# Kernel tuning notes

Measured on AMD Instinct MI355X. Metric: run time of the kernel, lower is better.

## Reference

```python
import jax, jax.numpy as jnp
import numpy as np

NEG_INF = -9e15
ALPHA = 0.2  # LeakyReLU negative slope

N, IN_F, OUT_F = 8192, 512, 64


def setup_inputs() -> dict:
    key = jax.random.key(0)
    k1, k2, k3, k4 = jax.random.split(key, 4)
    input = jax.random.normal(k1, (N, IN_F), dtype=jnp.float32)
    adj = jax.random.randint(k2, (N, N), 0, 2, dtype=jnp.int32)
    init_range = float(np.sqrt(6.0 / (IN_F + OUT_F)))
    W = jax.random.uniform(k3, (IN_F, OUT_F), dtype=jnp.float32,
                           minval=-init_range, maxval=init_range)
    a_range = float(np.sqrt(6.0 / (2 * OUT_F + 1)))
    a = jax.random.uniform(k4, (2 * OUT_F, 1), dtype=jnp.float32,
                           minval=-a_range, maxval=a_range)
    return {"input": input, "adj": adj, "W": W, "a": a}


def reference(input, adj, W, a):
    h = input @ W                      # [N, F']
    a_left, a_right = a[:OUT_F], a[OUT_F:]   # each [F', 1]
    att_l = h @ a_left                 # [N, 1]
    att_r = h @ a_right                # [N, 1]
    e = jax.nn.leaky_relu(att_l + att_r.T, negative_slope=ALPHA)  # [N, N]
    e = jnp.where(adj == 0, jnp.float32(NEG_INF), e)
    attention = jax.nn.softmax(e, axis=1)
    # dropout is identity in eval mode (training=False)
    h_prime = attention @ h            # [N, F']
    return jax.nn.elu(h_prime)         # concat=True -> ELU activation
```

## Files before the change

### kernel.cpp

```cpp
#include <hip/hip_runtime.h>
#include <stdint.h>

#define ALPHA 0.2f
#define LOG2E 1.44269504088896340736f

typedef __attribute__((ext_vector_type(8))) short bf16x8;
typedef __attribute__((ext_vector_type(4))) float f32x4;

__device__ __forceinline__ unsigned short f2bf(float f) {
    unsigned u = __builtin_bit_cast(unsigned, f);
    u += 0x7fffu + ((u >> 16) & 1u);
    return (unsigned short)(u >> 16);
}
__device__ __forceinline__ float bf2f(unsigned short h) {
    unsigned u = ((unsigned)h) << 16;
    return __builtin_bit_cast(float, u);
}
__device__ __forceinline__ unsigned f2ord(float f) {
    unsigned b = __builtin_bit_cast(unsigned, f);
    return (b & 0x80000000u) ? ~b : (b | 0x80000000u);
}
__device__ __forceinline__ float ord2f(unsigned k) {
    unsigned b = (k & 0x80000000u) ? (k & 0x7fffffffu) : ~k;
    return __builtin_bit_cast(float, b);
}

__global__ __launch_bounds__(256) void gat_pre(
    const float* __restrict__ input, const float* __restrict__ W,
    const float* __restrict__ a,
    float* __restrict__ attL, float* __restrict__ attR,
    unsigned short* __restrict__ hPack, unsigned* __restrict__ wsR)
{
    __shared__ float x_lds[16 * 512];
    __shared__ float h_lds[16 * 64];
    __shared__ unsigned rmax;
    const int tid = threadIdx.x;
    const int i0  = blockIdx.x * 16;
    if (tid == 0) rmax = 0u;

    {
        const float* src = input + (size_t)i0 * 512;
        #pragma unroll
        for (int u = 0; u < 8; ++u) {
            const int f = (u * 256 + tid) * 4;
            *(f32x4*)&x_lds[f] = *(const f32x4*)(src + f);
        }
    }
    __syncthreads();

    {
        const int c = tid & 63;
        const int w = tid >> 6;
        float acc[4] = {0.f, 0.f, 0.f, 0.f};
        const float* Wc = W + c;
        #pragma unroll 4
        for (int kk = 0; kk < 512; kk += 4) {
            const float w0 = Wc[(kk+0)*64], w1 = Wc[(kk+1)*64];
            const float w2 = Wc[(kk+2)*64], w3 = Wc[(kk+3)*64];
            #pragma unroll
            for (int ri = 0; ri < 4; ++ri) {
                const f32x4 x = *(const f32x4*)&x_lds[(w + 4*ri) * 512 + kk];
                acc[ri] += x.x * w0 + x.y * w1 + x.z * w2 + x.w * w3;
            }
        }
        #pragma unroll
        for (int ri = 0; ri < 4; ++ri)
            h_lds[(w + 4*ri) * 64 + c] = acc[ri];
    }
    __syncthreads();

    if (tid < 128) {
        const int row = tid >> 3;
        const int cs  = (tid & 7) * 8;
        float pL = 0.f, pR = 0.f;
        #pragma unroll
        for (int u = 0; u < 8; ++u) {
            const float hv = h_lds[row * 64 + cs + u];
            pL += hv * a[cs + u];
            pR += hv * a[64 + cs + u];
        }
        pL += __shfl_xor(pL, 1, 64); pR += __shfl_xor(pR, 1, 64);
        pL += __shfl_xor(pL, 2, 64); pR += __shfl_xor(pR, 2, 64);
        pL += __shfl_xor(pL, 4, 64); pR += __shfl_xor(pR, 4, 64);
        if ((tid & 7) == 0) {
            attL[i0 + row] = pL;
            attR[i0 + row] = pR;
            atomicMax(&rmax, f2ord(pR));
        }
    } else {
        const int t2   = tid - 128;
        const int g    = t2 >> 5;
        const int qq   = (t2 >> 4) & 1;
        const int m    = t2 & 15;
        const int jb   = blockIdx.x >> 1;
        const int half = blockIdx.x & 1;
        bf16x8 v;
        #pragma unroll
        for (int u = 0; u < 8; ++u)
            v[u] = (short)f2bf(h_lds[(qq * 8 + u) * 64 + g * 16 + m]);
        *(bf16x8*)&hPack[(size_t)(jb * 4 + g) * 512 + ((half * 2 + qq) * 16 + m) * 8] = v;
    }

    __syncthreads();
    if (tid == 0) atomicMax(wsR, rmax);
}

__global__ __launch_bounds__(256, 4) void gat_attn(
    const int* __restrict__ adj,
    const float* __restrict__ attL, const float* __restrict__ attR,
    const unsigned short* __restrict__ hPack, const unsigned* __restrict__ wsR,
    float* __restrict__ outAcc, float* __restrict__ lAcc)
{
    __shared__ unsigned smem[4096];
    __shared__ float l_lds[64];
    const int tid  = threadIdx.x;
    const int lane = tid & 63;
    const int wq   = tid >> 6;
    const int m    = lane & 15;
    const int quad = lane >> 4;
    const int ti   = blockIdx.x >> 2;
    const int q4   = blockIdx.x & 3;
    const int i0   = ti * 16;
    const int jc0  = q4 * 64 + wq * 16;

    {
        const int r    = tid >> 4;
        const int lidx = (tid & 3) * 16 + r;
        const int t    = (tid & 15) >> 2;
        unsigned char* bb = (unsigned char*)smem;
        const int* src = adj + (size_t)(i0 + r) * 8192 + q4 * 2048 + (tid & 15) * 8;
        #pragma unroll 4
        for (int it = 0; it < 16; ++it) {
            const int4 v0 = *(const int4*)(src + it * 128);
            const int4 v1 = *(const int4*)(src + it * 128 + 4);
            unsigned b = 0;
            b |= (v0.x != 0) << 0; b |= (v0.y != 0) << 1;
            b |= (v0.z != 0) << 2; b |= (v0.w != 0) << 3;
            b |= (v1.x != 0) << 4; b |= (v1.y != 0) << 5;
            b |= (v1.z != 0) << 6; b |= (v1.w != 0) << 7;
            bb[((((it >> 2) * 1024) + (it & 3) * 64 + lidx) << 2) + t] = (unsigned char)b;
        }
    }
    __syncthreads();

    unsigned abw[4];
    #pragma unroll
    for (int g4 = 0; g4 < 4; ++g4)
        abw[g4] = smem[wq * 1024 + g4 * 64 + lane];

    const float R   = ord2f(*wsR);
    const float a_l = attL[i0 + m];
    const float t0  = a_l + R;
    const float M   = fmaxf(t0, ALPHA * t0);
    const float mc  = M * LOG2E;

    const float*          ar_p = attR + jc0 * 32 + quad * 8;
    const unsigned short* hp_p = hPack + (size_t)jc0 * 4 * 512 + lane * 8;

    f32x4 acc[4];
    #pragma unroll
    for (int g = 0; g < 4; ++g) acc[g] = (f32x4){0.f, 0.f, 0.f, 0.f};
    float lsum = 0.f;

    #pragma unroll
    for (int jg = 0; jg < 4; ++jg) {
        const unsigned ab = abw[jg];
        #pragma unroll
        for (int t = 0; t < 4; ++t) {
            const int s = jg * 4 + t;
            const f32x4 r0 = *(const f32x4*)(ar_p + s * 32);
            const f32x4 r1 = *(const f32x4*)(ar_p + s * 32 + 4);
            bf16x8 B[4];
            #pragma unroll
            for (int g = 0; g < 4; ++g)
                B[g] = *(const bf16x8*)(hp_p + (size_t)(s * 4 + g) * 512);

            const unsigned bits = (ab >> (t * 8)) & 0xffu;
            const float tv[8] = { a_l + r0.x, a_l + r0.y, a_l + r0.z, a_l + r0.w,
                                  a_l + r1.x, a_l + r1.y, a_l + r1.z, a_l + r1.w };
            bf16x8 af;
            #pragma unroll
            for (int u = 0; u < 8; ++u) {
                const float e  = fmaxf(tv[u], ALPHA * tv[u]);
                const float pe = __builtin_amdgcn_exp2f(__builtin_fmaf(e, LOG2E, -mc));
                const float pv = (bits & (1u << u)) ? pe : 0.0f;
                const unsigned short pb = f2bf(pv);
                af[u] = (short)pb;
                lsum += bf2f(pb);
            }
            #pragma unroll
            for (int g = 0; g < 4; ++g)
                acc[g] = __builtin_amdgcn_mfma_f32_16x16x32_bf16(af, B[g], acc[g], 0, 0, 0);
        }
    }

    lsum += __shfl_xor(lsum, 16, 64);
    lsum += __shfl_xor(lsum, 32, 64);
    if (lane < 16) l_lds[wq * 16 + lane] = lsum;
    float* accf = (float*)smem;
    #pragma unroll
    for (int g = 0; g < 4; ++g)
        *(f32x4*)&accf[(wq * 64 + lane) * 16 + g * 4] = acc[g];
    __syncthreads();

    #pragma unroll
    for (int q = 0; q < 4; ++q) {
        const int e      = tid + q * 256;
        const int lane_e = e >> 4;
        const int k16    = e & 15;
        float s = 0.f;
        #pragma unroll
        for (int ww = 0; ww < 4; ++ww) s += accf[(ww * 64 + lane_e) * 16 + k16];
        const int row = (lane_e >> 4) * 4 + (k16 & 3);
        const int col = (k16 >> 2) * 16 + (lane_e & 15);
        unsafeAtomicAdd(&outAcc[(size_t)(i0 + row) * 64 + col], s);
    }
    if (tid < 16) {
        const float s = l_lds[tid] + l_lds[16 + tid] + l_lds[32 + tid] + l_lds[48 + tid];
        unsafeAtomicAdd(&lAcc[i0 + tid], s);
    }
}

__global__ __launch_bounds__(256) void gat_final(
    float* __restrict__ out, const float* __restrict__ lAcc)
{
    const int idx = blockIdx.x * 256 + threadIdx.x;
    const float v = out[idx] / lAcc[idx >> 6];
    out[idx] = v > 0.f ? v : (__builtin_amdgcn_exp2f(v * LOG2E) - 1.0f);
}

extern "C" void kernel_launch(void* const* d_in, const int* in_sizes, int n_in,
                              void* d_out, int out_size, void* d_ws, size_t ws_size,
                              hipStream_t stream) {
    const float* input = (const float*)d_in[0];
    const int*   adj   = (const int*)d_in[1];
    const float* W     = (const float*)d_in[2];
    const float* a     = (const float*)d_in[3];
    float* out = (float*)d_out;

    char* ws = (char*)d_ws;
    unsigned*       wsR   = (unsigned*)(ws + 0);
    float*          lAcc  = (float*)(ws + 4096);
    float*          attL  = (float*)(ws + 2134016);
    float*          attR  = (float*)(ws + 2166784);
    unsigned short* hPack = (unsigned short*)(ws + 2199552);

    hipMemsetAsync(d_out, 0, (size_t)out_size * sizeof(float), stream);
    hipMemsetAsync(d_ws, 0, 36864, stream);

    gat_pre  <<< 512, 256, 0, stream>>>(input, W, a, attL, attR, hPack, wsR);
    gat_attn <<<2048, 256, 0, stream>>>(adj, attL, attR, hPack, wsR, out, lAcc);
    gat_final<<<2048, 256, 0, stream>>>(out, lAcc);
}
```

Measured before the change: 419.3 us.

## Fuse normalization and ELU into attention kernel by giving each block full rows

Each attention block now processes all 8192 columns for its 16 rows using 8 waves, instead of splitting columns across 4 blocks. Partial results are reduced in LDS rather than with global atomics, and the softmax normalization and ELU are applied in place. This removes the output memset, the lAcc accumulator, the atomics and the separate final kernel. In exchange the grid has fewer, larger blocks and more registers per thread, which could reduce occupancy or cause spills under the 512x4 launch bound.

```diff
diff --git a/kernel.cpp b/kernel.cpp
--- a/kernel.cpp
+++ b/kernel.cpp
@@ -105,48 +105,49 @@
     if (tid == 0) atomicMax(wsR, rmax);
 }
 
-__global__ __launch_bounds__(256, 4) void gat_attn(
+__global__ __launch_bounds__(512, 4) void gat_attn(
     const int* __restrict__ adj,
     const float* __restrict__ attL, const float* __restrict__ attR,
     const unsigned short* __restrict__ hPack, const unsigned* __restrict__ wsR,
-    float* __restrict__ outAcc, float* __restrict__ lAcc)
+    float* __restrict__ out)
 {
-    __shared__ unsigned smem[4096];
-    __shared__ float l_lds[64];
+    __shared__ unsigned smem[8192];
+    __shared__ float l_lds[128];
     const int tid  = threadIdx.x;
     const int lane = tid & 63;
     const int wq   = tid >> 6;
     const int m    = lane & 15;
     const int quad = lane >> 4;
-    const int ti   = blockIdx.x >> 2;
-    const int q4   = blockIdx.x & 3;
-    const int i0   = ti * 16;
-    const int jc0  = q4 * 64 + wq * 16;
+    const int i0   = blockIdx.x * 16;
 
     {
-        const int r    = tid >> 4;
-        const int lidx = (tid & 3) * 16 + r;
-        const int t    = (tid & 15) >> 2;
+        const int r      = tid >> 5;
+        const int o      = tid & 31;
+        const int lane_s = (o & 3) * 16 + r;
+        const int tb     = (o >> 2) & 3;
+        const int gbase  = o >> 4;
         unsigned char* bb = (unsigned char*)smem;
-        const int* src = adj + (size_t)(i0 + r) * 8192 + q4 * 2048 + (tid & 15) * 8;
+        const int* src = adj + (size_t)(i0 + r) * 8192 + o * 8;
         #pragma unroll 4
-        for (int it = 0; it < 16; ++it) {
-            const int4 v0 = *(const int4*)(src + it * 128);
-            const int4 v1 = *(const int4*)(src + it * 128 + 4);
+        for (int it = 0; it < 32; ++it) {
+            const int4 v0 = *(const int4*)(src + it * 256);
+            const int4 v1 = *(const int4*)(src + it * 256 + 4);
             unsigned b = 0;
             b |= (v0.x != 0) << 0; b |= (v0.y != 0) << 1;
             b |= (v0.z != 0) << 2; b |= (v0.w != 0) << 3;
             b |= (v1.x != 0) << 4; b |= (v1.y != 0) << 5;
             b |= (v1.z != 0) << 6; b |= (v1.w != 0) << 7;
-            bb[((((it >> 2) * 1024) + (it & 3) * 64 + lidx) << 2) + t] = (unsigned char)b;
-        }
-    }
-    __syncthreads();
-
-    unsigned abw[4];
-    #pragma unroll
-    for (int g4 = 0; g4 < 4; ++g4)
-        abw[g4] = smem[wq * 1024 + g4 * 64 + lane];
+            const int idx = (it >> 2) * 512 + (gbase + (it & 3) * 2) * 64 + lane_s;
+            bb[(idx << 2) + tb] = (unsigned char)b;
+        }
+    }
+    __syncthreads();
+
+    unsigned abw[8];
+    #pragma unroll
+    for (int g = 0; g < 8; ++g)
+        abw[g] = smem[wq * 512 + g * 64 + lane];
+    __syncthreads();
 
     const float R   = ord2f(*wsR);
     const float a_l = attL[i0 + m];
@@ -154,6 +155,7 @@
     const float M   = fmaxf(t0, ALPHA * t0);
     const float mc  = M * LOG2E;
 
+    const int jc0 = wq * 32;
     const float*          ar_p = attR + jc0 * 32 + quad * 8;
     const unsigned short* hp_p = hPack + (size_t)jc0 * 4 * 512 + lane * 8;
 
@@ -163,7 +165,7 @@
     float lsum = 0.f;
 
     #pragma unroll
-    for (int jg = 0; jg < 4; ++jg) {
+    for (int jg = 0; jg < 8; ++jg) {
         const unsigned ab = abw[jg];
         #pragma unroll
         for (int t = 0; t < 4; ++t) {
@@ -204,29 +206,22 @@
     __syncthreads();
 
     #pragma unroll
-    for (int q = 0; q < 4; ++q) {
-        const int e      = tid + q * 256;
+    for (int q = 0; q < 2; ++q) {
+        const int e      = tid + q * 512;
         const int lane_e = e >> 4;
         const int k16    = e & 15;
         float s = 0.f;
         #pragma unroll
-        for (int ww = 0; ww < 4; ++ww) s += accf[(ww * 64 + lane_e) * 16 + k16];
+        for (int ww = 0; ww < 8; ++ww) s += accf[(ww * 64 + lane_e) * 16 + k16];
         const int row = (lane_e >> 4) * 4 + (k16 & 3);
         const int col = (k16 >> 2) * 16 + (lane_e & 15);
-        unsafeAtomicAdd(&outAcc[(size_t)(i0 + row) * 64 + col], s);
-    }
-    if (tid < 16) {
-        const float s = l_lds[tid] + l_lds[16 + tid] + l_lds[32 + tid] + l_lds[48 + tid];
-        unsafeAtomicAdd(&lAcc[i0 + tid], s);
-    }
-}
-
-__global__ __launch_bounds__(256) void gat_final(
-    float* __restrict__ out, const float* __restrict__ lAcc)
-{
-    const int idx = blockIdx.x * 256 + threadIdx.x;
-    const float v = out[idx] / lAcc[idx >> 6];
-    out[idx] = v > 0.f ? v : (__builtin_amdgcn_exp2f(v * LOG2E) - 1.0f);
+        float l = 0.f;
+        #pragma unroll
+        for (int ww = 0; ww < 8; ++ww) l += l_lds[ww * 16 + row];
+        const float v = s / l;
+        out[(size_t)(i0 + row) * 64 + col] =
+            v > 0.f ? v : (__builtin_amdgcn_exp2f(v * LOG2E) - 1.0f);
+    }
 }
 
 extern "C" void kernel_launch(void* const* d_in, const int* in_sizes, int n_in,
@@ -240,15 +235,12 @@
 
     char* ws = (char*)d_ws;
     unsigned*       wsR   = (unsigned*)(ws + 0);
-    float*          lAcc  = (float*)(ws + 4096);
     float*          attL  = (float*)(ws + 2134016);
     float*          attR  = (float*)(ws + 2166784);
     unsigned short* hPack = (unsigned short*)(ws + 2199552);
 
-    hipMemsetAsync(d_out, 0, (size_t)out_size * sizeof(float), stream);
-    hipMemsetAsync(d_ws, 0, 36864, stream);
+    hipMemsetAsync(d_ws, 0, 4096, stream);
 
     gat_pre  <<< 512, 256, 0, stream>>>(input, W, a, attL, attR, hPack, wsR);
-    gat_attn <<<2048, 256, 0, stream>>>(adj, attL, attR, hPack, wsR, out, lAcc);
-    gat_final<<<2048, 256, 0, stream>>>(out, lAcc);
-}
+    gat_attn <<< 512, 512, 0, stream>>>(adj, attL, attR, hPack, wsR, out);
+}
```

Measured after the change: 416.5 us. Within noise of the previous version (-0.7%).
